# Kernel optimization log

Hardware: AMD Instinct MI355X
Metric: run time of the kernel (lower is better)

## Reference

```python
import jax, jax.numpy as jnp
import numpy as np

EPS = 1e-5      # BatchNorm eps (torch default)
TEMP = 2.0      # initial_temperature
TOP_K = 2


def _bn(x, g, b, m, v):
    # eval-mode BatchNorm over channel dim of [B, C]
    return (x - m) * jax.lax.rsqrt(v + EPS) * g + b


def setup_inputs() -> dict:
    key = jax.random.key(0)
    ks = jax.random.split(key, 16)
    B, C, H, W, E = 64, 768, 32, 32, 16
    C2 = 2 * C            # 1536
    R = C2 // 16          # 96 (ChannelAttention bottleneck)
    s = 0.02
    f32 = jnp.float32
    return {
        "x": jax.random.normal(ks[0], (B, C, H, W), f32),
        # conv1x1 C->2C
        "w1": jax.random.normal(ks[1], (C2, C), f32) * s,
        "b1": jnp.zeros((C2,), f32),
        # BN(2C)
        "bn1_g": jnp.ones((C2,), f32),
        "bn1_b": jnp.zeros((C2,), f32),
        "bn1_m": jax.random.normal(ks[2], (C2,), f32) * 0.1,
        "bn1_v": jax.random.uniform(ks[3], (C2,), f32, 0.5, 1.5),
        # ChannelAttention fc: 2C -> 2C/16 -> 2C
        "caw1": jax.random.normal(ks[4], (R, C2), f32) * s,
        "cab1": jnp.zeros((R,), f32),
        "caw2": jax.random.normal(ks[5], (C2, R), f32) * s,
        "cab2": jnp.zeros((C2,), f32),
        # conv1x1 2C->C
        "w2": jax.random.normal(ks[6], (C, C2), f32) * s,
        "b2": jnp.zeros((C,), f32),
        # BN(C)
        "bn2_g": jnp.ones((C,), f32),
        "bn2_b": jnp.zeros((C,), f32),
        "bn2_m": jax.random.normal(ks[7], (C,), f32) * 0.1,
        "bn2_v": jax.random.uniform(ks[8], (C,), f32, 0.5, 1.5),
        # conv1x1 C->E
        "w3": jax.random.normal(ks[9], (E, C), f32) * s,
        "b3": jnp.zeros((E,), f32),
    }


def reference(x, w1, b1, bn1_g, bn1_b, bn1_m, bn1_v,
              caw1, cab1, caw2, cab2,
              w2, b2, bn2_g, bn2_b, bn2_m, bn2_v,
              w3, b3):
    # global avg pool: [B,C,H,W] -> [B,C] (1x1 spatial squeezed)
    g = jnp.mean(x, axis=(2, 3))
    # conv1x1 C->2C + BN + GELU (exact erf gelu, torch default)
    h = jax.nn.gelu(_bn(g @ w1.T + b1, bn1_g, bn1_b, bn1_m, bn1_v),
                    approximate=False)
    # ChannelAttention on 1x1 feature map: avg_pool == max_pool == identity,
    # so avg_out + max_out = 2 * fc(h)
    a = jax.nn.gelu(h @ caw1.T + cab1, approximate=False) @ caw2.T + cab2
    h = h * jax.nn.sigmoid(a + a)
    # conv1x1 2C->C + BN + GELU
    h = jax.nn.gelu(_bn(h @ w2.T + b2, bn2_g, bn2_b, bn2_m, bn2_v),
                    approximate=False)
    # conv1x1 C->E -> gating scores [B, E]
    scores = h @ w3.T + b3
    vals, idx = jax.lax.top_k(scores, TOP_K)
    probs = jax.nn.softmax(vals / TEMP, axis=1)
    return idx, probs
```

## Files before the change

kernel.cpp:

```cpp
#include <hip/hip_runtime.h>
#include <hip/hip_bf16.h>
#include <math.h>

#define B_   64
#define C_   768
#define C2_  1536
#define R_   96
#define E_   16
#define HW_  1024

__device__ __forceinline__ float gelu_exact(float x) {
    return 0.5f * x * (1.0f + erff(x * 0.70710678118654752440f));
}

__global__ __launch_bounds__(256) void pool_kernel(const float* __restrict__ x,
                                                   float* __restrict__ gT) {
    const int wave = threadIdx.x >> 6;
    const int lane = threadIdx.x & 63;
    const int row  = blockIdx.x * 4 + wave;
    const int b = row / C_;
    const int c = row % C_;
    const float4* p = reinterpret_cast<const float4*>(x + (size_t)row * HW_);
    float4 a0 = p[lane +   0];
    float4 a1 = p[lane +  64];
    float4 a2 = p[lane + 128];
    float4 a3 = p[lane + 192];
    float s = (a0.x + a0.y + a0.z + a0.w) + (a1.x + a1.y + a1.z + a1.w)
            + (a2.x + a2.y + a2.z + a2.w) + (a3.x + a3.y + a3.z + a3.w);
    #pragma unroll
    for (int off = 32; off >= 1; off >>= 1) s += __shfl_xor(s, off);
    if (lane == 0) gT[c * B_ + b] = s * (1.0f / (float)HW_);
}

template<int K, bool BN>
__global__ __launch_bounds__(512) void gemv2_kernel(
    const float* __restrict__ inT,
    const float* __restrict__ W,
    const float* __restrict__ bias,
    const float* __restrict__ bn_g, const float* __restrict__ bn_b,
    const float* __restrict__ bn_m, const float* __restrict__ bn_v,
    float* __restrict__ outT)
{
    __shared__ __align__(16) float wl[2 * K];
    __shared__ float part[2][8][64];
    const int t  = threadIdx.x;
    const int c0 = blockIdx.x * 2;
    {
        const float4* src = reinterpret_cast<const float4*>(W + (size_t)c0 * K);
        float4* dst = reinterpret_cast<float4*>(wl);
        #pragma unroll
        for (int i = t; i < K / 2; i += 512) dst[i] = src[i];
    }
    __syncthreads();
    const int b = t & 63, w = t >> 6;
    const int kc = w * (K / 8);
    const float* w0 = wl + kc;
    const float* w1 = wl + K + kc;
    const float* g  = inT + (size_t)kc * B_ + b;
    float a0 = 0.f, a1 = 0.f;
    #pragma unroll 16
    for (int k = 0; k < K / 8; ++k) {
        float gv = g[k * B_];
        a0 = fmaf(gv, w0[k], a0);
        a1 = fmaf(gv, w1[k], a1);
    }
    part[0][w][b] = a0;
    part[1][w][b] = a1;
    __syncthreads();
    if (t < 128) {
        const int ci = t >> 6, bb = t & 63, c = c0 + ci;
        float s = (part[ci][0][bb] + part[ci][1][bb])
                + (part[ci][2][bb] + part[ci][3][bb])
                + (part[ci][4][bb] + part[ci][5][bb])
                + (part[ci][6][bb] + part[ci][7][bb]);
        s += bias[c];
        if (BN) s = (s - bn_m[c]) * rsqrtf(bn_v[c] + 1e-5f) * bn_g[c] + bn_b[c];
        outT[(size_t)c * B_ + bb] = gelu_exact(s);
    }
}

__global__ __launch_bounds__(512) void gate_kernel(
    const float* __restrict__ rT,
    const float* __restrict__ caw2,
    const float* __restrict__ cab2,
    float* __restrict__ h1T)
{
    const int t = threadIdx.x;
    const int b = t & 63, w = t >> 6;
    const int c = blockIdx.x * 8 + w;
    const float* wr = caw2 + (size_t)c * R_;
    float acc = 0.f;
    #pragma unroll 12
    for (int k = 0; k < R_; ++k) acc = fmaf(rT[k * B_ + b], wr[k], acc);
    acc += cab2[c];
    float sig = 1.0f / (1.0f + expf(-2.0f * acc));
    h1T[(size_t)c * B_ + b] *= sig;
}

__global__ __launch_bounds__(256) void l5_kernel(
    const float* __restrict__ h2T, const float* __restrict__ w3,
    const float* __restrict__ b3, float* __restrict__ out)
{
    __shared__ __align__(16) float wl[E_ * C_];
    __shared__ float part[256];
    __shared__ float sc[E_];
    const int t = threadIdx.x;
    const int b = blockIdx.x;
    {
        const float4* src = reinterpret_cast<const float4*>(w3);
        float4* dst = reinterpret_cast<float4*>(wl);
        #pragma unroll
        for (int i = 0; i < 12; ++i) dst[t + 256 * i] = src[t + 256 * i];
    }
    __syncthreads();
    const int e = t & 15, kg = t >> 4;
    const float* wr = wl + e * C_ + kg * 48;
    const float* hv = h2T + (size_t)kg * 48 * B_ + b;
    float acc = 0.f;
    #pragma unroll 8
    for (int j = 0; j < 48; ++j) acc = fmaf(hv[j * B_], wr[j], acc);
    part[t] = acc;
    __syncthreads();
    if (t < E_) {
        float s = b3[t];
        #pragma unroll
        for (int kgi = 0; kgi < 16; ++kgi) s += part[kgi * 16 + t];
        sc[t] = s;
    }
    __syncthreads();
    if (t == 0) {
        int i0 = 0; float v0 = sc[0];
        #pragma unroll
        for (int i = 1; i < E_; ++i) { if (sc[i] > v0) { v0 = sc[i]; i0 = i; } }
        int i1 = -1; float v1 = -INFINITY;
        #pragma unroll
        for (int i = 0; i < E_; ++i) {
            if (i == i0) continue;
            if (sc[i] > v1) { v1 = sc[i]; i1 = i; }
        }
        float e1 = expf((v1 - v0) * 0.5f);
        float inv = 1.0f / (1.0f + e1);
        out[b * 2 + 0] = (float)i0;
        out[b * 2 + 1] = (float)i1;
        out[2 * B_ + b * 2 + 0] = inv;
        out[2 * B_ + b * 2 + 1] = e1 * inv;
    }
}

extern "C" void kernel_launch(void* const* d_in, const int* in_sizes, int n_in,
                              void* d_out, int out_size, void* d_ws, size_t ws_size,
                              hipStream_t stream) {
    const float* x     = (const float*)d_in[0];
    const float* w1    = (const float*)d_in[1];
    const float* b1    = (const float*)d_in[2];
    const float* bn1_g = (const float*)d_in[3];
    const float* bn1_b = (const float*)d_in[4];
    const float* bn1_m = (const float*)d_in[5];
    const float* bn1_v = (const float*)d_in[6];
    const float* caw1  = (const float*)d_in[7];
    const float* cab1  = (const float*)d_in[8];
    const float* caw2  = (const float*)d_in[9];
    const float* cab2  = (const float*)d_in[10];
    const float* w2    = (const float*)d_in[11];
    const float* b2    = (const float*)d_in[12];
    const float* bn2_g = (const float*)d_in[13];
    const float* bn2_b = (const float*)d_in[14];
    const float* bn2_m = (const float*)d_in[15];
    const float* bn2_v = (const float*)d_in[16];
    const float* w3    = (const float*)d_in[17];
    const float* b3    = (const float*)d_in[18];

    float* ws  = (float*)d_ws;
    float* gT  = ws;
    float* h1T = ws + 49152;
    float* rT  = ws + 49152 + 98304;
    float* h2T = ws + 49152 + 98304 + 6144;
    float* out = (float*)d_out;

    pool_kernel<<<(B_ * C_) / 4, 256, 0, stream>>>(x, gT);
    gemv2_kernel<C_, true><<<C2_ / 2, 512, 0, stream>>>(
        gT, w1, b1, bn1_g, bn1_b, bn1_m, bn1_v, h1T);
    gemv2_kernel<C2_, false><<<R_ / 2, 512, 0, stream>>>(
        h1T, caw1, cab1, nullptr, nullptr, nullptr, nullptr, rT);
    gate_kernel<<<C2_ / 8, 512, 0, stream>>>(rT, caw2, cab2, h1T);
    gemv2_kernel<C2_, true><<<C_ / 2, 512, 0, stream>>>(
        h1T, w2, b2, bn2_g, bn2_b, bn2_m, bn2_v, h2T);
    l5_kernel<<<B_, 256, 0, stream>>>(h2T, w3, b3, out);
}
```

Before: 72.22 us.

## Fuse post-pool GEMV chain into one persistent kernel with grid barriers

```diff
diff --git a/kernel.cpp b/kernel.cpp
--- a/kernel.cpp
+++ b/kernel.cpp
@@ -8,13 +8,28 @@
 #define R_   96
 #define E_   16
 #define HW_  1024
+#define GRID_ 256
+#define THR_  512
 
 __device__ __forceinline__ float gelu_exact(float x) {
     return 0.5f * x * (1.0f + erff(x * 0.70710678118654752440f));
 }
 
+__device__ __forceinline__ void grid_barrier(unsigned* ctr, unsigned target) {
+    __syncthreads();
+    if (threadIdx.x == 0) {
+        __hip_atomic_fetch_add(ctr, 1u, __ATOMIC_ACQ_REL, __HIP_MEMORY_SCOPE_AGENT);
+        while (__hip_atomic_load(ctr, __ATOMIC_ACQUIRE, __HIP_MEMORY_SCOPE_AGENT) < target)
+            __builtin_amdgcn_s_sleep(2);
+    }
+    __syncthreads();
+}
+
 __global__ __launch_bounds__(256) void pool_kernel(const float* __restrict__ x,
-                                                   float* __restrict__ gT) {
+                                                   float* __restrict__ gT,
+                                                   unsigned* __restrict__ ctr) {
+    if (blockIdx.x == 0 && threadIdx.x == 0)
+        __hip_atomic_store(ctr, 0u, __ATOMIC_RELAXED, __HIP_MEMORY_SCOPE_AGENT);
     const int wave = threadIdx.x >> 6;
     const int lane = threadIdx.x & 63;
     const int row  = blockIdx.x * 4 + wave;
@@ -32,118 +47,195 @@
     if (lane == 0) gT[c * B_ + b] = s * (1.0f / (float)HW_);
 }
 
-template<int K, bool BN>
-__global__ __launch_bounds__(512) void gemv2_kernel(
-    const float* __restrict__ inT,
-    const float* __restrict__ W,
-    const float* __restrict__ bias,
-    const float* __restrict__ bn_g, const float* __restrict__ bn_b,
-    const float* __restrict__ bn_m, const float* __restrict__ bn_v,
-    float* __restrict__ outT)
+__global__ __launch_bounds__(512) void fused_chain(
+    const float* __restrict__ gT,
+    const float* __restrict__ w1, const float* __restrict__ b1,
+    const float* __restrict__ bn1_g, const float* __restrict__ bn1_b,
+    const float* __restrict__ bn1_m, const float* __restrict__ bn1_v,
+    const float* __restrict__ caw1, const float* __restrict__ cab1,
+    const float* __restrict__ caw2, const float* __restrict__ cab2,
+    const float* __restrict__ w2, const float* __restrict__ b2,
+    const float* __restrict__ bn2_g, const float* __restrict__ bn2_b,
+    const float* __restrict__ bn2_m, const float* __restrict__ bn2_v,
+    const float* __restrict__ w3, const float* __restrict__ b3,
+    float* __restrict__ h1T, float* __restrict__ rT, float* __restrict__ h2T,
+    float* __restrict__ out, unsigned* __restrict__ ctr)
 {
-    __shared__ __align__(16) float wl[2 * K];
-    __shared__ float part[2][8][64];
-    const int t  = threadIdx.x;
-    const int c0 = blockIdx.x * 2;
+    __shared__ float smem[13456];
+    const int t   = threadIdx.x;
+    const int bid = blockIdx.x;
+    const int b   = t & 63;
+    const int w   = t >> 6;
+
     {
-        const float4* src = reinterpret_cast<const float4*>(W + (size_t)c0 * K);
+        float* wl   = smem;
+        float* part = smem + 4608;
+        const int c0 = bid * 6;
+        const float4* src = reinterpret_cast<const float4*>(w1 + (size_t)c0 * C_);
         float4* dst = reinterpret_cast<float4*>(wl);
         #pragma unroll
-        for (int i = t; i < K / 2; i += 512) dst[i] = src[i];
-    }
-    __syncthreads();
-    const int b = t & 63, w = t >> 6;
-    const int kc = w * (K / 8);
-    const float* w0 = wl + kc;
-    const float* w1 = wl + K + kc;
-    const float* g  = inT + (size_t)kc * B_ + b;
-    float a0 = 0.f, a1 = 0.f;
-    #pragma unroll 16
-    for (int k = 0; k < K / 8; ++k) {
-        float gv = g[k * B_];
-        a0 = fmaf(gv, w0[k], a0);
-        a1 = fmaf(gv, w1[k], a1);
-    }
-    part[0][w][b] = a0;
-    part[1][w][b] = a1;
-    __syncthreads();
-    if (t < 128) {
-        const int ci = t >> 6, bb = t & 63, c = c0 + ci;
-        float s = (part[ci][0][bb] + part[ci][1][bb])
-                + (part[ci][2][bb] + part[ci][3][bb])
-                + (part[ci][4][bb] + part[ci][5][bb])
-                + (part[ci][6][bb] + part[ci][7][bb]);
-        s += bias[c];
-        if (BN) s = (s - bn_m[c]) * rsqrtf(bn_v[c] + 1e-5f) * bn_g[c] + bn_b[c];
-        outT[(size_t)c * B_ + bb] = gelu_exact(s);
-    }
-}
-
-__global__ __launch_bounds__(512) void gate_kernel(
-    const float* __restrict__ rT,
-    const float* __restrict__ caw2,
-    const float* __restrict__ cab2,
-    float* __restrict__ h1T)
-{
-    const int t = threadIdx.x;
-    const int b = t & 63, w = t >> 6;
-    const int c = blockIdx.x * 8 + w;
-    const float* wr = caw2 + (size_t)c * R_;
-    float acc = 0.f;
-    #pragma unroll 12
-    for (int k = 0; k < R_; ++k) acc = fmaf(rT[k * B_ + b], wr[k], acc);
-    acc += cab2[c];
-    float sig = 1.0f / (1.0f + expf(-2.0f * acc));
-    h1T[(size_t)c * B_ + b] *= sig;
-}
-
-__global__ __launch_bounds__(256) void l5_kernel(
-    const float* __restrict__ h2T, const float* __restrict__ w3,
-    const float* __restrict__ b3, float* __restrict__ out)
-{
-    __shared__ __align__(16) float wl[E_ * C_];
-    __shared__ float part[256];
-    __shared__ float sc[E_];
-    const int t = threadIdx.x;
-    const int b = blockIdx.x;
+        for (int i = 0; i < 3; ++i) {
+            int idx = t + i * THR_;
+            if (idx < 1152) dst[idx] = src[idx];
+        }
+        __syncthreads();
+        const int kc = w * 96;
+        float acc[6] = {0.f, 0.f, 0.f, 0.f, 0.f, 0.f};
+        const float* gp = gT + (size_t)kc * B_ + b;
+        #pragma unroll 8
+        for (int k = 0; k < 96; ++k) {
+            float gv = gp[k * B_];
+            #pragma unroll
+            for (int j = 0; j < 6; ++j)
+                acc[j] = fmaf(gv, wl[j * C_ + kc + k], acc[j]);
+        }
+        #pragma unroll
+        for (int j = 0; j < 6; ++j) part[j * 512 + w * 64 + b] = acc[j];
+        __syncthreads();
+        if (t < 384) {
+            const int ci = t >> 6, bb = t & 63, c = c0 + ci;
+            float s = 0.f;
+            #pragma unroll
+            for (int ww = 0; ww < 8; ++ww) s += part[ci * 512 + ww * 64 + bb];
+            s += b1[c];
+            s = (s - bn1_m[c]) * rsqrtf(bn1_v[c] + 1e-5f) * bn1_g[c] + bn1_b[c];
+            h1T[(size_t)c * B_ + bb] = gelu_exact(s);
+        }
+    }
+    grid_barrier(ctr, GRID_);
+
+    if (bid < R_) {
+        float* wl   = smem;
+        float* part = smem + C2_;
+        const float4* src = reinterpret_cast<const float4*>(caw1 + (size_t)bid * C2_);
+        float4* dst = reinterpret_cast<float4*>(wl);
+        if (t < 384) dst[t] = src[t];
+        __syncthreads();
+        const int kc = w * 192;
+        float a0 = 0.f, a1 = 0.f;
+        const float* hp = h1T + (size_t)kc * B_ + b;
+        #pragma unroll 8
+        for (int k = 0; k < 96; ++k) {
+            a0 = fmaf(hp[k * B_],        wl[kc + k],      a0);
+            a1 = fmaf(hp[(k + 96) * B_], wl[kc + k + 96], a1);
+        }
+        part[w * 64 + b] = a0 + a1;
+        __syncthreads();
+        if (t < 64) {
+            float s = 0.f;
+            #pragma unroll
+            for (int ww = 0; ww < 8; ++ww) s += part[ww * 64 + t];
+            rT[(size_t)bid * B_ + t] = gelu_exact(s + cab1[bid]);
+        }
+    }
+    grid_barrier(ctr, 2 * GRID_);
+
     {
-        const float4* src = reinterpret_cast<const float4*>(w3);
+        const int c0 = bid * 6;
+        if (w < 6) {
+            const int c = c0 + w;
+            const float* wr = caw2 + (size_t)c * R_;
+            const float* rp = rT + b;
+            float a0 = 0.f, a1 = 0.f;
+            #pragma unroll 8
+            for (int k = 0; k < 48; ++k) {
+                a0 = fmaf(rp[k * B_],        wr[k],      a0);
+                a1 = fmaf(rp[(k + 48) * B_], wr[k + 48], a1);
+            }
+            float a = a0 + a1 + cab2[c];
+            float sig = 1.0f / (1.0f + expf(-2.0f * a));
+            h1T[(size_t)c * B_ + b] *= sig;
+        }
+    }
+    grid_barrier(ctr, 3 * GRID_);
+
+    {
+        float* wl   = smem;
+        float* part = smem + 4608;
+        const int c0 = bid * 3;
+        const float4* src = reinterpret_cast<const float4*>(w2 + (size_t)c0 * C2_);
         float4* dst = reinterpret_cast<float4*>(wl);
         #pragma unroll
-        for (int i = 0; i < 12; ++i) dst[t + 256 * i] = src[t + 256 * i];
-    }
-    __syncthreads();
-    const int e = t & 15, kg = t >> 4;
-    const float* wr = wl + e * C_ + kg * 48;
-    const float* hv = h2T + (size_t)kg * 48 * B_ + b;
-    float acc = 0.f;
-    #pragma unroll 8
-    for (int j = 0; j < 48; ++j) acc = fmaf(hv[j * B_], wr[j], acc);
-    part[t] = acc;
-    __syncthreads();
-    if (t < E_) {
-        float s = b3[t];
-        #pragma unroll
-        for (int kgi = 0; kgi < 16; ++kgi) s += part[kgi * 16 + t];
-        sc[t] = s;
-    }
-    __syncthreads();
-    if (t == 0) {
-        int i0 = 0; float v0 = sc[0];
-        #pragma unroll
-        for (int i = 1; i < E_; ++i) { if (sc[i] > v0) { v0 = sc[i]; i0 = i; } }
-        int i1 = -1; float v1 = -INFINITY;
-        #pragma unroll
-        for (int i = 0; i < E_; ++i) {
-            if (i == i0) continue;
-            if (sc[i] > v1) { v1 = sc[i]; i1 = i; }
-        }
-        float e1 = expf((v1 - v0) * 0.5f);
-        float inv = 1.0f / (1.0f + e1);
-        out[b * 2 + 0] = (float)i0;
-        out[b * 2 + 1] = (float)i1;
-        out[2 * B_ + b * 2 + 0] = inv;
-        out[2 * B_ + b * 2 + 1] = e1 * inv;
+        for (int i = 0; i < 3; ++i) {
+            int idx = t + i * THR_;
+            if (idx < 1152) dst[idx] = src[idx];
+        }
+        __syncthreads();
+        const int kc = w * 192;
+        float acc0[3] = {0.f, 0.f, 0.f};
+        float acc1[3] = {0.f, 0.f, 0.f};
+        const float* hp = h1T + (size_t)kc * B_ + b;
+        #pragma unroll 4
+        for (int k = 0; k < 96; ++k) {
+            float h0  = hp[k * B_];
+            float h1v = hp[(k + 96) * B_];
+            #pragma unroll
+            for (int j = 0; j < 3; ++j) {
+                acc0[j] = fmaf(h0,  wl[j * C2_ + kc + k],      acc0[j]);
+                acc1[j] = fmaf(h1v, wl[j * C2_ + kc + k + 96], acc1[j]);
+            }
+        }
+        #pragma unroll
+        for (int j = 0; j < 3; ++j) part[j * 512 + w * 64 + b] = acc0[j] + acc1[j];
+        __syncthreads();
+        if (t < 192) {
+            const int ci = t >> 6, bb = t & 63, c = c0 + ci;
+            float s = 0.f;
+            #pragma unroll
+            for (int ww = 0; ww < 8; ++ww) s += part[ci * 512 + ww * 64 + bb];
+            s += b2[c];
+            s = (s - bn2_m[c]) * rsqrtf(bn2_v[c] + 1e-5f) * bn2_g[c] + bn2_b[c];
+            h2T[(size_t)c * B_ + bb] = gelu_exact(s);
+        }
+    }
+    grid_barrier(ctr, 4 * GRID_);
+
+    if (bid < B_) {
+        float* w3l  = smem;
+        float* h2l  = smem + 12304;
+        float* part = smem + 13072;
+        float* sc   = smem + 13328;
+        const int bb = bid;
+        #pragma unroll
+        for (int e = 0; e < E_; ++e)
+            for (int i = t; i < C_; i += THR_)
+                w3l[e * 769 + i] = w3[e * C_ + i];
+        for (int k = t; k < C_; k += THR_) h2l[k] = h2T[(size_t)k * B_ + bb];
+        __syncthreads();
+        if (t < 256) {
+            const int e = t & 15, kg = t >> 4;
+            const float* wr = w3l + e * 769 + kg * 48;
+            const float* hv = h2l + kg * 48;
+            float acc = 0.f;
+            #pragma unroll 8
+            for (int j = 0; j < 48; ++j) acc = fmaf(hv[j], wr[j], acc);
+            part[t] = acc;
+        }
+        __syncthreads();
+        if (t < E_) {
+            float s = b3[t];
+            #pragma unroll
+            for (int kg = 0; kg < 16; ++kg) s += part[kg * 16 + t];
+            sc[t] = s;
+        }
+        __syncthreads();
+        if (t == 0) {
+            int i0 = 0; float v0 = sc[0];
+            #pragma unroll
+            for (int i = 1; i < E_; ++i) { if (sc[i] > v0) { v0 = sc[i]; i0 = i; } }
+            int i1 = -1; float v1 = -INFINITY;
+            #pragma unroll
+            for (int i = 0; i < E_; ++i) {
+                if (i == i0) continue;
+                if (sc[i] > v1) { v1 = sc[i]; i1 = i; }
+            }
+            float e1 = expf((v1 - v0) * 0.5f);
+            float inv = 1.0f / (1.0f + e1);
+            out[bb * 2 + 0] = (float)i0;
+            out[bb * 2 + 1] = (float)i1;
+            out[2 * B_ + bb * 2 + 0] = inv;
+            out[2 * B_ + bb * 2 + 1] = e1 * inv;
+        }
     }
 }
 
@@ -173,17 +265,15 @@
     float* ws  = (float*)d_ws;
     float* gT  = ws;
     float* h1T = ws + 49152;
-    float* rT  = ws + 49152 + 98304;
-    float* h2T = ws + 49152 + 98304 + 6144;
+    float* rT  = ws + 147456;
+    float* h2T = ws + 153600;
+    unsigned* ctr = (unsigned*)(ws + 202752);
     float* out = (float*)d_out;
 
-    pool_kernel<<<(B_ * C_) / 4, 256, 0, stream>>>(x, gT);
-    gemv2_kernel<C_, true><<<C2_ / 2, 512, 0, stream>>>(
-        gT, w1, b1, bn1_g, bn1_b, bn1_m, bn1_v, h1T);
-    gemv2_kernel<C2_, false><<<R_ / 2, 512, 0, stream>>>(
-        h1T, caw1, cab1, nullptr, nullptr, nullptr, nullptr, rT);
-    gate_kernel<<<C2_ / 8, 512, 0, stream>>>(rT, caw2, cab2, h1T);
-    gemv2_kernel<C2_, true><<<C_ / 2, 512, 0, stream>>>(
-        h1T, w2, b2, bn2_g, bn2_b, bn2_m, bn2_v, h2T);
-    l5_kernel<<<B_, 256, 0, stream>>>(h2T, w3, b3, out);
-}
+    pool_kernel<<<(B_ * C_) / 4, 256, 0, stream>>>(x, gT, ctr);
+    fused_chain<<<GRID_, THR_, 0, stream>>>(
+        gT, w1, b1, bn1_g, bn1_b, bn1_m, bn1_v,
+        caw1, cab1, caw2, cab2,
+        w2, b2, bn2_g, bn2_b, bn2_m, bn2_v,
+        w3, b3, h1T, rT, h2T, out, ctr);
+}
```

New measurement: 139.0 us. +92.5%, slower.

## Fuse caw1 projection into layer-1 GEMV via atomics and restructure gate and w2 kernels

Applied to the files above, without the earlier changes.

```diff
diff --git a/kernel.cpp b/kernel.cpp
--- a/kernel.cpp
+++ b/kernel.cpp
@@ -9,22 +9,30 @@
 #define E_   16
 #define HW_  1024
 
+typedef float f32x4 __attribute__((ext_vector_type(4)));
+
 __device__ __forceinline__ float gelu_exact(float x) {
     return 0.5f * x * (1.0f + erff(x * 0.70710678118654752440f));
 }
 
 __global__ __launch_bounds__(256) void pool_kernel(const float* __restrict__ x,
-                                                   float* __restrict__ gT) {
+                                                   float* __restrict__ gT,
+                                                   float* __restrict__ r_pre) {
+    if (blockIdx.x == 0) {
+        #pragma unroll
+        for (int i = 0; i < (R_ * B_) / 256; ++i)
+            r_pre[i * 256 + threadIdx.x] = 0.0f;
+    }
     const int wave = threadIdx.x >> 6;
     const int lane = threadIdx.x & 63;
     const int row  = blockIdx.x * 4 + wave;
     const int b = row / C_;
     const int c = row % C_;
-    const float4* p = reinterpret_cast<const float4*>(x + (size_t)row * HW_);
-    float4 a0 = p[lane +   0];
-    float4 a1 = p[lane +  64];
-    float4 a2 = p[lane + 128];
-    float4 a3 = p[lane + 192];
+    const f32x4* p = reinterpret_cast<const f32x4*>(x + (size_t)row * HW_);
+    f32x4 a0 = __builtin_nontemporal_load(p + lane +   0);
+    f32x4 a1 = __builtin_nontemporal_load(p + lane +  64);
+    f32x4 a2 = __builtin_nontemporal_load(p + lane + 128);
+    f32x4 a3 = __builtin_nontemporal_load(p + lane + 192);
     float s = (a0.x + a0.y + a0.z + a0.w) + (a1.x + a1.y + a1.z + a1.w)
             + (a2.x + a2.y + a2.z + a2.w) + (a3.x + a3.y + a3.z + a3.w);
     #pragma unroll
@@ -32,69 +40,155 @@
     if (lane == 0) gT[c * B_ + b] = s * (1.0f / (float)HW_);
 }
 
-template<int K, bool BN>
-__global__ __launch_bounds__(512) void gemv2_kernel(
-    const float* __restrict__ inT,
-    const float* __restrict__ W,
-    const float* __restrict__ bias,
+__global__ __launch_bounds__(512) void l1r_kernel(
+    const float* __restrict__ gT,
+    const float* __restrict__ w1, const float* __restrict__ b1,
     const float* __restrict__ bn_g, const float* __restrict__ bn_b,
     const float* __restrict__ bn_m, const float* __restrict__ bn_v,
-    float* __restrict__ outT)
-{
-    __shared__ __align__(16) float wl[2 * K];
+    const float* __restrict__ caw1,
+    float* __restrict__ h1T, float* __restrict__ r_pre)
+{
+    __shared__ __align__(16) float wl[6 * C_];
+    __shared__ float part[6][8][64];
+    __shared__ float hl[6][64];
+    const int t  = threadIdx.x;
+    const int c0 = blockIdx.x * 6;
+    {
+        const float4* src = reinterpret_cast<const float4*>(w1 + (size_t)c0 * C_);
+        float4* dst = reinterpret_cast<float4*>(wl);
+        #pragma unroll
+        for (int i = 0; i < 3; ++i) {
+            int idx = t + i * 512;
+            if (idx < 1152) dst[idx] = src[idx];
+        }
+    }
+    __syncthreads();
+    const int b = t & 63, w = t >> 6;
+    const int kc = w * 96;
+    float acc[6] = {0.f, 0.f, 0.f, 0.f, 0.f, 0.f};
+    const float* gp = gT + (size_t)kc * B_ + b;
+    #pragma unroll 8
+    for (int k = 0; k < 96; ++k) {
+        float gv = gp[k * B_];
+        #pragma unroll
+        for (int j = 0; j < 6; ++j)
+            acc[j] = fmaf(gv, wl[j * C_ + kc + k], acc[j]);
+    }
+    #pragma unroll
+    for (int j = 0; j < 6; ++j) part[j][w][b] = acc[j];
+    __syncthreads();
+    if (t < 384) {
+        const int ci = t >> 6, bb = t & 63, c = c0 + ci;
+        float s = 0.f;
+        #pragma unroll
+        for (int ww = 0; ww < 8; ++ww) s += part[ci][ww][bb];
+        s += b1[c];
+        s = (s - bn_m[c]) * rsqrtf(bn_v[c] + 1e-5f) * bn_g[c] + bn_b[c];
+        float h = gelu_exact(s);
+        h1T[(size_t)c * B_ + bb] = h;
+        hl[ci][bb] = h;
+    }
+    __syncthreads();
+    if (t < 192) {
+        const int j = t % 96, half = t / 96;
+        float cw[6];
+        #pragma unroll
+        for (int ci = 0; ci < 6; ++ci) cw[ci] = caw1[(size_t)j * C2_ + c0 + ci];
+        float* rp = r_pre + j * B_ + half * 32;
+        #pragma unroll 4
+        for (int bb = 0; bb < 32; ++bb) {
+            float v = 0.f;
+            #pragma unroll
+            for (int ci = 0; ci < 6; ++ci) v = fmaf(cw[ci], hl[ci][half * 32 + bb], v);
+            atomicAdd(&rp[bb], v);
+        }
+    }
+}
+
+__global__ __launch_bounds__(512) void gate_kernel(
+    const float* __restrict__ r_pre, const float* __restrict__ cab1,
+    const float* __restrict__ caw2, const float* __restrict__ cab2,
+    const float* __restrict__ h1T, float* __restrict__ h1gT)
+{
+    __shared__ __align__(16) float rl[R_ * B_];
+    const int t = threadIdx.x;
+    {
+        const float4* src = reinterpret_cast<const float4*>(r_pre);
+        float4* dst = reinterpret_cast<float4*>(rl);
+        #pragma unroll
+        for (int i = 0; i < 3; ++i) {
+            int idx = t + i * 512;
+            float4 v = src[idx];
+            float cb = cab1[idx >> 4];
+            v.x = gelu_exact(v.x + cb);
+            v.y = gelu_exact(v.y + cb);
+            v.z = gelu_exact(v.z + cb);
+            v.w = gelu_exact(v.w + cb);
+            dst[idx] = v;
+        }
+    }
+    __syncthreads();
+    const int b = t & 63, w = t >> 6;
+    const int c = blockIdx.x * 8 + w;
+    const int cu = __builtin_amdgcn_readfirstlane(c);
+    const float* wr = caw2 + (size_t)cu * R_;
+    float a0 = 0.f, a1 = 0.f;
+    #pragma unroll 8
+    for (int k = 0; k < 48; ++k) {
+        a0 = fmaf(rl[k * B_ + b],        wr[k],      a0);
+        a1 = fmaf(rl[(k + 48) * B_ + b], wr[k + 48], a1);
+    }
+    float a = a0 + a1 + cab2[cu];
+    float sig = 1.0f / (1.0f + expf(-2.0f * a));
+    h1gT[(size_t)cu * B_ + b] = h1T[(size_t)cu * B_ + b] * sig;
+}
+
+__global__ __launch_bounds__(512) void l4_kernel(
+    const float* __restrict__ h1gT, const float* __restrict__ w2,
+    const float* __restrict__ b2,
+    const float* __restrict__ bn_g, const float* __restrict__ bn_b,
+    const float* __restrict__ bn_m, const float* __restrict__ bn_v,
+    float* __restrict__ h2T)
+{
+    __shared__ __align__(16) float wl[2 * C2_];
     __shared__ float part[2][8][64];
     const int t  = threadIdx.x;
     const int c0 = blockIdx.x * 2;
     {
-        const float4* src = reinterpret_cast<const float4*>(W + (size_t)c0 * K);
+        const float4* src = reinterpret_cast<const float4*>(w2 + (size_t)c0 * C2_);
         float4* dst = reinterpret_cast<float4*>(wl);
         #pragma unroll
-        for (int i = t; i < K / 2; i += 512) dst[i] = src[i];
+        for (int i = 0; i < 2; ++i) {
+            int idx = t + i * 512;
+            if (idx < 768) dst[idx] = src[idx];
+        }
     }
     __syncthreads();
     const int b = t & 63, w = t >> 6;
-    const int kc = w * (K / 8);
-    const float* w0 = wl + kc;
-    const float* w1 = wl + K + kc;
-    const float* g  = inT + (size_t)kc * B_ + b;
-    float a0 = 0.f, a1 = 0.f;
-    #pragma unroll 16
-    for (int k = 0; k < K / 8; ++k) {
-        float gv = g[k * B_];
-        a0 = fmaf(gv, w0[k], a0);
-        a1 = fmaf(gv, w1[k], a1);
-    }
-    part[0][w][b] = a0;
-    part[1][w][b] = a1;
+    const int kc = w * 192;
+    float a00 = 0.f, a01 = 0.f, a10 = 0.f, a11 = 0.f;
+    const float* hp = h1gT + (size_t)kc * B_ + b;
+    #pragma unroll 8
+    for (int k = 0; k < 96; ++k) {
+        float h0 = hp[k * B_];
+        float h1 = hp[(k + 96) * B_];
+        a00 = fmaf(h0, wl[kc + k],            a00);
+        a01 = fmaf(h1, wl[kc + k + 96],       a01);
+        a10 = fmaf(h0, wl[C2_ + kc + k],      a10);
+        a11 = fmaf(h1, wl[C2_ + kc + k + 96], a11);
+    }
+    part[0][w][b] = a00 + a01;
+    part[1][w][b] = a10 + a11;
     __syncthreads();
     if (t < 128) {
         const int ci = t >> 6, bb = t & 63, c = c0 + ci;
-        float s = (part[ci][0][bb] + part[ci][1][bb])
-                + (part[ci][2][bb] + part[ci][3][bb])
-                + (part[ci][4][bb] + part[ci][5][bb])
-                + (part[ci][6][bb] + part[ci][7][bb]);
-        s += bias[c];
-        if (BN) s = (s - bn_m[c]) * rsqrtf(bn_v[c] + 1e-5f) * bn_g[c] + bn_b[c];
-        outT[(size_t)c * B_ + bb] = gelu_exact(s);
-    }
-}
-
-__global__ __launch_bounds__(512) void gate_kernel(
-    const float* __restrict__ rT,
-    const float* __restrict__ caw2,
-    const float* __restrict__ cab2,
-    float* __restrict__ h1T)
-{
-    const int t = threadIdx.x;
-    const int b = t & 63, w = t >> 6;
-    const int c = blockIdx.x * 8 + w;
-    const float* wr = caw2 + (size_t)c * R_;
-    float acc = 0.f;
-    #pragma unroll 12
-    for (int k = 0; k < R_; ++k) acc = fmaf(rT[k * B_ + b], wr[k], acc);
-    acc += cab2[c];
-    float sig = 1.0f / (1.0f + expf(-2.0f * acc));
-    h1T[(size_t)c * B_ + b] *= sig;
+        float s = 0.f;
+        #pragma unroll
+        for (int ww = 0; ww < 8; ++ww) s += part[ci][ww][bb];
+        s += b2[c];
+        s = (s - bn_m[c]) * rsqrtf(bn_v[c] + 1e-5f) * bn_g[c] + bn_b[c];
+        h2T[(size_t)c * B_ + bb] = gelu_exact(s);
+    }
 }
 
 __global__ __launch_bounds__(256) void l5_kernel(
@@ -170,20 +264,20 @@
     const float* w3    = (const float*)d_in[17];
     const float* b3    = (const float*)d_in[18];
 
-    float* ws  = (float*)d_ws;
-    float* gT  = ws;
-    float* h1T = ws + 49152;
-    float* rT  = ws + 49152 + 98304;
-    float* h2T = ws + 49152 + 98304 + 6144;
+    float* ws    = (float*)d_ws;
+    float* gT    = ws;
+    float* h1T   = ws + 49152;
+    float* r_pre = ws + 147456;
+    float* h2T   = ws + 153600;
+    float* h1gT  = ws + 202752;
     float* out = (float*)d_out;
 
-    pool_kernel<<<(B_ * C_) / 4, 256, 0, stream>>>(x, gT);
-    gemv2_kernel<C_, true><<<C2_ / 2, 512, 0, stream>>>(
-        gT, w1, b1, bn1_g, bn1_b, bn1_m, bn1_v, h1T);
-    gemv2_kernel<C2_, false><<<R_ / 2, 512, 0, stream>>>(
-        h1T, caw1, cab1, nullptr, nullptr, nullptr, nullptr, rT);
-    gate_kernel<<<C2_ / 8, 512, 0, stream>>>(rT, caw2, cab2, h1T);
-    gemv2_kernel<C2_, true><<<C_ / 2, 512, 0, stream>>>(
-        h1T, w2, b2, bn2_g, bn2_b, bn2_m, bn2_v, h2T);
+    pool_kernel<<<(B_ * C_) / 4, 256, 0, stream>>>(x, gT, r_pre);
+    l1r_kernel<<<C2_ / 6, 512, 0, stream>>>(
+        gT, w1, b1, bn1_g, bn1_b, bn1_m, bn1_v, caw1, h1T, r_pre);
+    gate_kernel<<<C2_ / 8, 512, 0, stream>>>(
+        r_pre, cab1, caw2, cab2, h1T, h1gT);
+    l4_kernel<<<C_ / 2, 512, 0, stream>>>(
+        h1gT, w2, b2, bn2_g, bn2_b, bn2_m, bn2_v, h2T);
     l5_kernel<<<B_, 256, 0, stream>>>(h2T, w3, b3, out);
 }
```

Result: slower. 165.7 us (+129.5%).
